# Kernel tuning notes

Hardware: AMD Instinct MI355X
Metric: run time of the kernel (lower is better)

Reference implementation:

```python
import math
import jax, jax.numpy as jnp
import numpy as np

E = 1024   # embed_dim
H = 16     # num_heads
DH = E // H
EPS = 1e-8

def round_ste(x):
    # straight-through round (matches brevitas STE behavior)
    return x + jax.lax.stop_gradient(jnp.round(x) - x)

def _scale(x, qmax):
    # dynamic per-tensor abs-max scale (stand-in for brevitas calibrated scale)
    return jnp.maximum(jnp.max(jnp.abs(x)) / qmax, EPS)

def fq(x, s, qmin, qmax):
    # fake-quantize: quantize to int grid, dequantize back to float
    return jnp.clip(round_ste(x / s), qmin, qmax) * s

def quant_linear(x, W, b):
    # Int8ActPerTensorFloat input, Int8WeightPerTensorFloat (narrow range) weight, Int32Bias
    s_x = _scale(x, 128.0)
    s_w = _scale(W, 127.0)
    xq = fq(x, s_x, -128, 127)
    wq = fq(W, s_w, -127, 127)
    y = xq @ wq.T
    if b is not None:
        s_b = s_x * s_w
        y = y + round_ste(b / s_b) * s_b
    return y

def setup_inputs() -> dict:
    k = jax.random.key(0)
    ks = jax.random.split(k, 7)
    S, B = 1024, 4
    return {
        "query": jax.random.normal(ks[0], (S, B, E), jnp.float32),
        "key": jax.random.normal(ks[1], (S, B, E), jnp.float32),
        "value": jax.random.normal(ks[2], (S, B, E), jnp.float32),
        "in_proj_weight": jax.random.normal(ks[3], (3 * E, E), jnp.float32) * 0.02,
        "in_proj_bias": jax.random.normal(ks[4], (3 * E,), jnp.float32) * 0.02,
        "out_proj_weight": jax.random.normal(ks[5], (E, E), jnp.float32) * 0.02,
        "out_proj_bias": jax.random.normal(ks[6], (E,), jnp.float32) * 0.02,
    }

def reference(query, key, value, in_proj_weight, in_proj_bias, out_proj_weight, out_proj_bias):
    S, B, _ = query.shape
    Wq, Wk, Wv = jnp.split(in_proj_weight, 3, axis=0)
    bq, bk, bv = jnp.split(in_proj_bias, 3)
    # quantized QKV projections (packed in_proj split per-input)
    q = quant_linear(query, Wq, bq)   # (S,B,E)
    k = quant_linear(key, Wk, bk)
    v = quant_linear(value, Wv, bv)

    def to_heads(x):  # (S,B,E) -> (B*H, S, DH)
        return x.reshape(S, B * H, DH).transpose(1, 0, 2)

    q = to_heads(q)
    k = to_heads(k)
    v = to_heads(v)

    # q_scaled quant (int8)
    q = q / math.sqrt(DH)
    q = fq(q, _scale(q, 128.0), -128, 127)
    # k_transposed quant (int8)
    kt = k.transpose(0, 2, 1)  # (B*H, DH, S)
    kt = fq(kt, _scale(kt, 128.0), -128, 127)

    attn = q @ kt                      # (B*H, S, S); softmax_input_quant=None -> identity
    attn = jax.nn.softmax(attn, axis=-1)
    # attn_output_weights quant (uint8)
    s_a = jnp.maximum(jnp.max(attn) / 255.0, EPS)
    attn = jnp.clip(round_ste(attn / s_a), 0, 255) * s_a
    # v quant (int8)
    v = fq(v, _scale(v, 128.0), -128, 127)

    out = attn @ v                     # (B*H, S, DH)
    out = out.transpose(1, 0, 2).reshape(S, B, E)
    out = quant_linear(out, out_proj_weight, out_proj_bias)
    return out
```

## Files before the change

### kernel.cpp

```cpp
#include <hip/hip_runtime.h>
#include <stdint.h>

typedef unsigned short u16;
typedef signed char i8;
typedef unsigned char u8;
typedef __attribute__((ext_vector_type(8))) short bf16x8;
typedef __attribute__((ext_vector_type(4))) float f32x4;
typedef __attribute__((ext_vector_type(4))) int i32x4;

#define S_LEN 1024
#define BATCH 4
#define EMB   1024
#define NH    16
#define DHEAD 64
#define BHEAD 64
#define NTOK  4096
#define KDIM  1024
#define NDIM  1024
#define EPSF  1e-8f
#define LOG2E 1.4426950408889634f

#define MFMAI8(a,b,c)  __builtin_amdgcn_mfma_i32_16x16x64_i8((a),(b),(c),0,0,0)

#define GLOAD16(g, l) __builtin_amdgcn_global_load_lds( \
    (const __attribute__((address_space(1))) void*)(g), \
    (__attribute__((address_space(3))) void*)(l), 16, 0, 0)

#define EXP2F(x) __builtin_amdgcn_exp2f(x)

__device__ __forceinline__ unsigned pack4(float a, float b, float c, float d){
  int qa = (int)a, qb = (int)b, qc = (int)c, qd = (int)d;
  return (unsigned)(qa & 255) | ((unsigned)(qb & 255) << 8) |
         ((unsigned)(qc & 255) << 16) | ((unsigned)(qd & 255) << 24);
}

__device__ __forceinline__ float wave_max(float v){
#pragma unroll
  for (int off = 32; off > 0; off >>= 1) v = fmaxf(v, __shfl_xor(v, off));
  return v;
}


__global__ __launch_bounds__(256) void k_zero(float* sc, int* vtot){
  if (blockIdx.x == 0){
    if (threadIdx.x < 16) sc[threadIdx.x] = 0.0f;
  } else {
    vtot[(blockIdx.x - 1)*256 + threadIdx.x] = 0;
  }
}

struct AQDesc { const float* x; u8* y; int n4; int slot; float qdiv; float lo; };
struct AQTable { AQDesc d[7]; };

__global__ __launch_bounds__(256) void k_absmax7(AQTable t, int* __restrict__ sci){
  const int bid = blockIdx.x;
  int seg, b0, nb;
  if (bid < 1536){ seg = bid >> 9; b0 = seg << 9; nb = 512; }
  else { seg = 3 + ((bid - 1536) >> 7); b0 = 1536 + ((seg - 3) << 7); nb = 128; }
  const AQDesc D = t.d[seg];
  float m = 0.0f;
  const float4* x4 = (const float4*)D.x;
  for (int i = (bid - b0)*256 + threadIdx.x; i < D.n4; i += nb*256){
    float4 v = x4[i];
    m = fmaxf(m, fmaxf(fmaxf(fabsf(v.x), fabsf(v.y)), fmaxf(fabsf(v.z), fabsf(v.w))));
  }
  m = wave_max(m);
  __shared__ float red[4];
  int lane = threadIdx.x & 63, w = threadIdx.x >> 6;
  if (lane == 0) red[w] = m;
  __syncthreads();
  if (threadIdx.x == 0){
    float mm = fmaxf(fmaxf(red[0], red[1]), fmaxf(red[2], red[3]));
    atomicMax(sci + D.slot, __float_as_int(mm));
  }
}

__global__ __launch_bounds__(256) void k_quant7(AQTable t, const float* __restrict__ sc){
  const int bid = blockIdx.x;
  int seg, b0, nb;
  if (bid < 1536){ seg = bid >> 9; b0 = seg << 9; nb = 512; }
  else { seg = 3 + ((bid - 1536) >> 7); b0 = 1536 + ((seg - 3) << 7); nb = 128; }
  const AQDesc D = t.d[seg];
  const float s = fmaxf(sc[D.slot] / D.qdiv, EPSF);
  const float lo = D.lo;
  const float4* x4 = (const float4*)D.x;
  unsigned* y4 = (unsigned*)D.y;
  for (int i = (bid - b0)*256 + threadIdx.x; i < D.n4; i += nb*256){
    float4 v = x4[i];
    float t0 = fminf(fmaxf(rintf(v.x / s), lo), 127.f);
    float t1 = fminf(fmaxf(rintf(v.y / s), lo), 127.f);
    float t2 = fminf(fmaxf(rintf(v.z / s), lo), 127.f);
    float t3 = fminf(fmaxf(rintf(v.w / s), lo), 127.f);
    y4[i] = pack4(t0, t1, t2, t3);
  }
}

__global__ __launch_bounds__(256) void k_quant(const float* __restrict__ x,
    u8* __restrict__ y, int n4, const float* __restrict__ sc, int slot){
  const float s = fmaxf(sc[slot] / 128.0f, EPSF);
  const float4* x4 = (const float4*)x;
  unsigned* y4 = (unsigned*)y;
  for (int i = blockIdx.x*256 + threadIdx.x; i < n4; i += gridDim.x*256){
    float4 v = x4[i];
    float t0 = fminf(fmaxf(rintf(v.x / s), -128.f), 127.f);
    float t1 = fminf(fmaxf(rintf(v.y / s), -128.f), 127.f);
    float t2 = fminf(fmaxf(rintf(v.z / s), -128.f), 127.f);
    float t3 = fminf(fmaxf(rintf(v.w / s), -128.f), 127.f);
    y4[i] = pack4(t0, t1, t2, t3);
  }
}

__device__ __forceinline__ void gemm_body(const i8* __restrict__ A,
    const i8* __restrict__ W, const float* __restrict__ bias,
    float* __restrict__ out, float s_b, int rowBase, int colBase,
    int* __restrict__ amax_out, i8 (*As)[128], i8 (*Bs)[128], float* red){
  const int tid = threadIdx.x;
  const int wid = tid >> 6, lane = tid & 63;
  const int wm = wid >> 2, wn = wid & 3;
  const int rr = lane & 15, g = lane >> 4;
  const int srow = wid*8 + (lane >> 3);
  const int sco  = ((lane & 7) ^ (lane >> 3)) << 4;
  const i8* Arow0 = &A[(size_t)(rowBase + srow)*KDIM + sco];
  const i8* Arow1 = &A[(size_t)(rowBase + 64 + srow)*KDIM + sco];
  const i8* Wrow0 = &W[(size_t)(colBase + srow)*KDIM + sco];
  const i8* Wrow1 = &W[(size_t)(colBase + 64 + srow)*KDIM + sco];
  i32x4 c[4][2] = {};
  int aoff[4][2], boff[2][2];
#pragma unroll
  for (int i = 0; i < 4; i++){
    int row = wm*64 + i*16 + rr;
#pragma unroll
    for (int h = 0; h < 2; h++)
      aoff[i][h] = row*128 + (((h*4 + g) ^ (row & 7)) << 4);
  }
#pragma unroll
  for (int j = 0; j < 2; j++){
    int row = wn*32 + j*16 + rr;
#pragma unroll
    for (int h = 0; h < 2; h++)
      boff[j][h] = row*128 + (((h*4 + g) ^ (row & 7)) << 4);
  }
  for (int k0 = 0; k0 < KDIM; k0 += 128){
    __syncthreads();
    GLOAD16(Arow0 + k0, &As[wid*8][0]);
    GLOAD16(Arow1 + k0, &As[64 + wid*8][0]);
    GLOAD16(Wrow0 + k0, &Bs[wid*8][0]);
    GLOAD16(Wrow1 + k0, &Bs[64 + wid*8][0]);
    __syncthreads();
#pragma unroll
    for (int h = 0; h < 2; h++){
      i32x4 af[4], bfr[2];
#pragma unroll
      for (int i = 0; i < 4; i++) af[i]  = *(const i32x4*)((const i8*)As + aoff[i][h]);
#pragma unroll
      for (int j = 0; j < 2; j++) bfr[j] = *(const i32x4*)((const i8*)Bs + boff[j][h]);
#pragma unroll
      for (int i = 0; i < 4; i++)
#pragma unroll
        for (int j = 0; j < 2; j++)
          c[i][j] = MFMAI8(af[i], bfr[j], c[i][j]);
    }
  }
  float lmax = 0.0f;
  const int r0 = (lane >> 4) * 4, ccol = lane & 15;
#pragma unroll
  for (int j = 0; j < 2; j++){
    int col = colBase + wn*32 + j*16 + ccol;
    float rb = rintf(bias[col] / s_b);
#pragma unroll
    for (int i = 0; i < 4; i++){
      int rowb = rowBase + wm*64 + i*16 + r0;
#pragma unroll
      for (int rI = 0; rI < 4; rI++){
        float y = s_b * ((float)c[i][j][rI] + rb);
        out[(size_t)(rowb + rI)*NDIM + col] = y;
        lmax = fmaxf(lmax, fabsf(y));
      }
    }
  }
  lmax = wave_max(lmax);
  if (lane == 0) red[wid] = lmax;
  __syncthreads();
  if (tid == 0){
    float mm = red[0];
#pragma unroll
    for (int i2 = 1; i2 < 8; i2++) mm = fmaxf(mm, red[i2]);
    atomicMax(amax_out, __float_as_int(mm));
  }
}

__global__ __launch_bounds__(512) void k_gemm3(const i8* __restrict__ Xall,
    const i8* __restrict__ Wall, const float* __restrict__ ball,
    float* __restrict__ Yall, const float* __restrict__ sc, int* __restrict__ sci){
  __shared__ i8 As[128][128];
  __shared__ i8 Bs[128][128];
  __shared__ float red[8];
  const int orig = blockIdx.x;
  const int xcd = orig & 7, sl = orig >> 3;
  const int seg = sl >> 5;
  const int t2 = xcd*32 + (sl & 31);
  const int by = t2 >> 3, bx = t2 & 7;
  const float s_x = fmaxf(sc[seg] / 128.0f, EPSF);
  const float s_w = fmaxf(sc[3 + seg] / 127.0f, EPSF);
  gemm_body(Xall + (size_t)seg*NTOK*KDIM, Wall + (size_t)seg*KDIM*NDIM,
            ball + seg*1024, Yall + (size_t)seg*NTOK*NDIM, s_x*s_w,
            by*128, bx*128, sci + 7 + seg, As, Bs, red);
}

__global__ __launch_bounds__(512) void k_gemm1(const i8* __restrict__ A,
    const i8* __restrict__ W, const float* __restrict__ bias,
    float* __restrict__ out, const float* __restrict__ sc,
    int sx_slot, int sw_slot, int* __restrict__ amax_out){
  __shared__ i8 As[128][128];
  __shared__ i8 Bs[128][128];
  __shared__ float red[8];
  const int orig = blockIdx.x;
  const int t2 = (orig & 7)*32 + (orig >> 3);
  const int by = t2 >> 3, bx = t2 & 7;
  const float s_x = fmaxf(sc[sx_slot] / 128.0f, EPSF);
  const float s_w = fmaxf(sc[sw_slot] / 127.0f, EPSF);
  gemm_body(A, W, bias, out, s_x*s_w, by*128, bx*128, amax_out, As, Bs, red);
}

__global__ __launch_bounds__(256) void k_quant_heads(const float* __restrict__ qf,
    const float* __restrict__ kf, const float* __restrict__ vf,
    i8* __restrict__ qh, i8* __restrict__ kh, i8* __restrict__ vt,
    int* __restrict__ vtot, const float* __restrict__ sc){
  const float s_q = fmaxf((sc[7]*0.125f)/128.0f, EPSF);
  const float s_k = fmaxf(sc[8]/128.0f, EPSF);
  const float s_v = fmaxf(sc[9]/128.0f, EPSF);
  __shared__ i8 tile[64][68];
  const int bx = blockIdx.x;
  const int st = bx & 15, hh = (bx >> 4) & 15, b = bx >> 8;
  const int t = threadIdx.x;
  const int sl = t >> 2, dc = (t & 3) * 16;
  const size_t row = (size_t)(st*64 + sl)*BATCH + b;
  const size_t ibase = row*EMB + hh*DHEAD + dc;
  const int bh = b*NH + hh;
  float vq[16], vk[16], vv[16];
#pragma unroll
  for (int i = 0; i < 4; i++){
    *(float4*)&vq[i*4] = *(const float4*)&qf[ibase + i*4];
    *(float4*)&vk[i*4] = *(const float4*)&kf[ibase + i*4];
    *(float4*)&vv[i*4] = *(const float4*)&vf[ibase + i*4];
  }
  alignas(16) i8 oq[16], ok[16];
#pragma unroll
  for (int i = 0; i < 16; i++){
    float tq = fminf(fmaxf(rintf((vq[i]*0.125f)/s_q), -128.f), 127.f);
    float tk = fminf(fmaxf(rintf(vk[i]/s_k), -128.f), 127.f);
    float tv = fminf(fmaxf(rintf(vv[i]/s_v), -128.f), 127.f);
    oq[i] = (i8)(int)tq; ok[i] = (i8)(int)tk;
    tile[dc + i][sl] = (i8)(int)tv;
  }
  const size_t qoff = ((size_t)bh*S_LEN + st*64 + sl)*DHEAD + dc;
  *(int4*)&qh[qoff] = *(const int4*)&oq[0];
  *(int4*)&kh[qoff] = *(const int4*)&ok[0];
  __syncthreads();
  const int d = t >> 2, sc4 = (t & 3) * 16;
  int ovi[4];
  int sum = 0;
#pragma unroll
  for (int w4 = 0; w4 < 4; w4++){
    unsigned x = *(const unsigned*)&tile[d][sc4 + w4*4];
    ovi[w4] = (int)x;
#pragma unroll
    for (int bb = 0; bb < 4; bb++) sum += (int)(i8)(x >> (8*bb));
  }
  const size_t voff = ((size_t)bh*DHEAD + d)*S_LEN + st*64 + sc4;
  *(int4*)&vt[voff] = *(const int4*)&ovi[0];
  sum += __shfl_xor(sum, 1);
  sum += __shfl_xor(sum, 2);
  if ((t & 3) == 0) atomicAdd(&vtot[bh*DHEAD + d], sum);
}

__global__ __launch_bounds__(256) void k_attn1(const i8* __restrict__ qh,
    const i8* __restrict__ kh, float* __restrict__ mrow, float* __restrict__ lrow,
    const float* __restrict__ sc, int* __restrict__ sci){
  __shared__ i8 Ks[64][64];
  __shared__ float red2[4];
  const int orig = blockIdx.x;
  const int tile = (orig & 7) * 128 + (orig >> 3);
  const int bhead = tile >> 4, q0 = (tile & 15) * 64;
  const int tid = threadIdx.x, w = tid >> 6, lane = tid & 63;
  const int rr = lane & 15, g = lane >> 4;
  const float s_q = fmaxf((sc[7]*0.125f)/128.0f, EPSF);
  const float s_k = fmaxf(sc[8]/128.0f, EPSF);
  const float C1 = s_q * s_k * LOG2E;
  const i8* qbase = qh + ((size_t)bhead*S_LEN + q0 + w*16)*DHEAD;
  const i8* kbase = kh + (size_t)bhead*S_LEN*DHEAD;
  i32x4 a = *(const i32x4*)&qbase[rr*DHEAD + g*16];
  const int srow = w*16 + (lane >> 2);
  const int sco  = ((lane & 3) ^ ((srow >> 1) & 3)) << 4;
  float m[4] = {-1e30f, -1e30f, -1e30f, -1e30f};
  float l[4] = {0.f, 0.f, 0.f, 0.f};
  for (int cch = 0; cch < 16; cch++){
    const int n0 = cch * 64;
    __syncthreads();
    GLOAD16(&kbase[(size_t)(n0 + srow)*DHEAD + sco], &Ks[w*16][0]);
    __syncthreads();
    float sv[4][4];
#pragma unroll
    for (int nt = 0; nt < 4; nt++){
      int row = nt*16 + rr;
      i32x4 b = *(const i32x4*)((const i8*)Ks + row*64 + (((g ^ ((row >> 1) & 3))) << 4));
      i32x4 acc = {};
      acc = MFMAI8(a, b, acc);
#pragma unroll
      for (int r = 0; r < 4; r++) sv[nt][r] = (float)acc[r]*C1;
    }
#pragma unroll
    for (int r = 0; r < 4; r++){
      float cm = fmaxf(fmaxf(sv[0][r], sv[1][r]), fmaxf(sv[2][r], sv[3][r]));
      float mn = fmaxf(m[r], cm);
      l[r] *= EXP2F(m[r] - mn);
      m[r] = mn;
#pragma unroll
      for (int nt = 0; nt < 4; nt++)
        l[r] += EXP2F(sv[nt][r] - m[r]);
    }
  }
#pragma unroll
  for (int off = 1; off < 16; off <<= 1){
#pragma unroll
    for (int r = 0; r < 4; r++){
      float mo = __shfl_xor(m[r], off), lo = __shfl_xor(l[r], off);
      float mn = fmaxf(m[r], mo);
      l[r] = l[r]*EXP2F(m[r] - mn) + lo*EXP2F(mo - mn);
      m[r] = mn;
    }
  }
  if (rr == 0){
    int rowb = q0 + w*16 + g*4;
#pragma unroll
    for (int r = 0; r < 4; r++){
      mrow[(size_t)bhead*S_LEN + rowb + r] = m[r];
      lrow[(size_t)bhead*S_LEN + rowb + r] = l[r];
    }
  }
  float im = 0.0f;
#pragma unroll
  for (int r = 0; r < 4; r++) im = fmaxf(im, 1.0f / l[r]);
  im = wave_max(im);
  if (lane == 0) red2[w] = im;
  __syncthreads();
  if (tid == 0){
    float mm = fmaxf(fmaxf(red2[0], red2[1]), fmaxf(red2[2], red2[3]));
    atomicMax(sci + 13, __float_as_int(mm));
  }
}

__global__ __launch_bounds__(256) void k_attn2(const i8* __restrict__ qh,
    const i8* __restrict__ kh, const i8* __restrict__ vt,
    const float* __restrict__ mrow, const float* __restrict__ lrow,
    const int* __restrict__ vtot, float* __restrict__ aout,
    const float* __restrict__ sc, const int* __restrict__ sci,
    int* __restrict__ amax_out){
  __shared__ i8 Ks[64][64];
  __shared__ i8 Vs[64][64];
  __shared__ i8 P[4][16][68];
  __shared__ float red[4];
  const int orig = blockIdx.x;
  const int tile = (orig & 7) * 128 + (orig >> 3);
  const int bhead = tile >> 4, q0 = (tile & 15) * 64;
  const int tid = threadIdx.x, w = tid >> 6, lane = tid & 63;
  const int rr = lane & 15, g = lane >> 4;
  const float s_q = fmaxf((sc[7]*0.125f)/128.0f, EPSF);
  const float s_k = fmaxf(sc[8]/128.0f, EPSF);
  const float C1 = s_q * s_k * LOG2E;
  const float s_v = fmaxf(sc[9]/128.0f, EPSF);
  const float s_a = fmaxf(__int_as_float(sci[13]) / 255.0f, EPSF);
  const float fac = s_a * s_v;
  const i8* qbase = qh + ((size_t)bhead*S_LEN + q0 + w*16)*DHEAD;
  const i8* kbase = kh + (size_t)bhead*S_LEN*DHEAD;
  const i8* vbase = vt + (size_t)bhead*DHEAD*S_LEN;
  i32x4 a = *(const i32x4*)&qbase[rr*DHEAD + g*16];
  float nm[4], inv[4];
  {
    int rowb = q0 + w*16 + g*4;
#pragma unroll
    for (int r = 0; r < 4; r++){
      nm[r]  = -mrow[(size_t)bhead*S_LEN + rowb + r];
      inv[r] = 1.0f / (lrow[(size_t)bhead*S_LEN + rowb + r] * s_a);
    }
  }
  const int srow = w*16 + (lane >> 2);
  const int sco  = ((lane & 3) ^ ((srow >> 1) & 3)) << 4;
  const int vco  = (lane & 3) << 4;
  i32x4 cpv[4] = {};
  for (int cch = 0; cch < 16; cch++){
    const int n0 = cch * 64;
    __syncthreads();
    GLOAD16(&kbase[(size_t)(n0 + srow)*DHEAD + sco], &Ks[w*16][0]);
    GLOAD16(&vbase[(size_t)srow*S_LEN + n0 + vco], &Vs[w*16][0]);
    __syncthreads();
#pragma unroll
    for (int nt = 0; nt < 4; nt++){
      int row = nt*16 + rr;
      i32x4 b = *(const i32x4*)((const i8*)Ks + row*64 + (((g ^ ((row >> 1) & 3))) << 4));
      i32x4 acc = {};
      acc = MFMAI8(a, b, acc);
#pragma unroll
      for (int r = 0; r < 4; r++){
        float arg = fmaf((float)acc[r], C1, nm[r]);
        float e   = EXP2F(arg);
        float pq  = fminf(rintf(e * inv[r]), 255.0f);
        P[w][g*4 + r][nt*16 + rr] = (i8)((int)pq - 128);
      }
    }
    i32x4 pa;
    {
      const i8* pptr = &P[w][rr][g*16];
      pa[0] = *(const int*)(pptr + 0);
      pa[1] = *(const int*)(pptr + 4);
      pa[2] = *(const int*)(pptr + 8);
      pa[3] = *(const int*)(pptr + 12);
    }
#pragma unroll
    for (int f = 0; f < 4; f++){
      i32x4 bv = *(const i32x4*)&Vs[f*16 + rr][g*16];
      cpv[f] = MFMAI8(pa, bv, cpv[f]);
    }
  }
  const int b = bhead >> 4, hh = bhead & 15;
  float lmax = 0.0f;
#pragma unroll
  for (int f = 0; f < 4; f++){
    int d = f*16 + rr;
    int vcorr = 128 * vtot[bhead*DHEAD + d];
#pragma unroll
    for (int r = 0; r < 4; r++){
      int srow2 = q0 + w*16 + g*4 + r;
      float y = fac * (float)(cpv[f][r] + vcorr);
      aout[(size_t)(srow2*BATCH + b)*EMB + hh*DHEAD + d] = y;
      lmax = fmaxf(lmax, fabsf(y));
    }
  }
  lmax = wave_max(lmax);
  __syncthreads();
  if (lane == 0) red[w] = lmax;
  __syncthreads();
  if (tid == 0){
    float mm = fmaxf(fmaxf(red[0], red[1]), fmaxf(red[2], red[3]));
    atomicMax(amax_out, __float_as_int(mm));
  }
}

extern "C" void kernel_launch(void* const* d_in, const int* in_sizes, int n_in,
                              void* d_out, int out_size, void* d_ws, size_t ws_size,
                              hipStream_t stream){
  const float* query = (const float*)d_in[0];
  const float* key   = (const float*)d_in[1];
  const float* value = (const float*)d_in[2];
  const float* inW   = (const float*)d_in[3];
  const float* inB   = (const float*)d_in[4];
  const float* outW  = (const float*)d_in[5];
  const float* outB  = (const float*)d_in[6];
  float* out = (float*)d_out;

  char* ws = (char*)d_ws;
  float* sc  = (float*)ws;
  int*   sci = (int*)ws;
  int*   vtotI = (int*)(ws + 256);
  u8* WQQ = (u8*)(ws + 256 + 16384);
  u8* WKQ = WQQ + 1024*1024;
  u8* WVQ = WKQ + 1024*1024;
  u8* WOQ = WVQ + 1024*1024;
  u8* XQ  = WOQ + 1024*1024;
  u8* XK  = XQ + (size_t)NTOK*1024;
  u8* XV  = XK + (size_t)NTOK*1024;
  float* QF = (float*)(XV + (size_t)NTOK*1024);
  float* KF = QF + (size_t)NTOK*1024;
  float* VF = KF + (size_t)NTOK*1024;
  i8* VT = (i8*)(VF + (size_t)NTOK*1024);
  float* MROW = (float*)(VT + (size_t)BHEAD*DHEAD*S_LEN);
  float* LROW = MROW + BHEAD*S_LEN;
  i8* QH  = (i8*)XQ;   i8* KH = (i8*)XK;
  float* AOUT = QF;
  u8* AOQ = XV;

  AQTable tab;
  tab.d[0] = { query,             XQ,  NTOK*1024/4, 0, 128.f, -128.f };
  tab.d[1] = { key,               XK,  NTOK*1024/4, 1, 128.f, -128.f };
  tab.d[2] = { value,             XV,  NTOK*1024/4, 2, 128.f, -128.f };
  tab.d[3] = { inW,               WQQ, 1024*1024/4, 3, 127.f, -127.f };
  tab.d[4] = { inW + 1024*1024,   WKQ, 1024*1024/4, 4, 127.f, -127.f };
  tab.d[5] = { inW + 2*1024*1024, WVQ, 1024*1024/4, 5, 127.f, -127.f };
  tab.d[6] = { outW,              WOQ, 1024*1024/4, 6, 127.f, -127.f };

  k_zero<<<17, 256, 0, stream>>>(sc, vtotI);
  k_absmax7<<<2048, 256, 0, stream>>>(tab, sci);
  k_quant7<<<2048, 256, 0, stream>>>(tab, sc);
  k_gemm3<<<768, 512, 0, stream>>>((const i8*)XQ, (const i8*)WQQ, inB, QF, sc, sci);
  k_quant_heads<<<1024, 256, 0, stream>>>(QF, KF, VF, QH, KH, VT, vtotI, sc);
  k_attn1<<<1024, 256, 0, stream>>>(QH, KH, MROW, LROW, sc, sci);
  k_attn2<<<1024, 256, 0, stream>>>(QH, KH, VT, MROW, LROW, vtotI, AOUT, sc, sci, sci + 10);
  k_quant<<<1024, 256, 0, stream>>>(AOUT, AOQ, NTOK*1024/4, sc, 10);
  k_gemm1<<<256, 512, 0, stream>>>((const i8*)AOQ, (const i8*)WOQ, outB, out, sc, 10, 6, sci + 12);
}
```

Baseline: 191.6 us.

## Transpose QK MFMA operands so each lane owns one query row, pack P writes

The attention kernels swap the MFMA operand order so each lane holds scores for a single query row. Softmax stats then reduce across lane groups with shuffles instead of keeping four rows per lane. In the second pass, the normalization is folded into the exp2 bias via log2(inv). The four uint8 probabilities are packed into one 32-bit shared store with a single XOR for the offset, and the V tile in LDS gets an XOR swizzle to reduce bank conflicts. The exp-then-scale is approximated by exp2 with a log-folded bias, which could shift rounding slightly at the quantization edges.

```diff
diff --git a/kernel.cpp b/kernel.cpp
--- a/kernel.cpp
+++ b/kernel.cpp
@@ -292,8 +292,7 @@
   i32x4 a = *(const i32x4*)&qbase[rr*DHEAD + g*16];
   const int srow = w*16 + (lane >> 2);
   const int sco  = ((lane & 3) ^ ((srow >> 1) & 3)) << 4;
-  float m[4] = {-1e30f, -1e30f, -1e30f, -1e30f};
-  float l[4] = {0.f, 0.f, 0.f, 0.f};
+  float m = -1e30f, l = 0.0f;
   for (int cch = 0; cch < 16; cch++){
     const int n0 = cch * 64;
     __syncthreads();
@@ -305,43 +304,35 @@
       int row = nt*16 + rr;
       i32x4 b = *(const i32x4*)((const i8*)Ks + row*64 + (((g ^ ((row >> 1) & 3))) << 4));
       i32x4 acc = {};
-      acc = MFMAI8(a, b, acc);
+      acc = MFMAI8(b, a, acc);
 #pragma unroll
       for (int r = 0; r < 4; r++) sv[nt][r] = (float)acc[r]*C1;
     }
-#pragma unroll
-    for (int r = 0; r < 4; r++){
-      float cm = fmaxf(fmaxf(sv[0][r], sv[1][r]), fmaxf(sv[2][r], sv[3][r]));
-      float mn = fmaxf(m[r], cm);
-      l[r] *= EXP2F(m[r] - mn);
-      m[r] = mn;
-#pragma unroll
-      for (int nt = 0; nt < 4; nt++)
-        l[r] += EXP2F(sv[nt][r] - m[r]);
-    }
-  }
-#pragma unroll
-  for (int off = 1; off < 16; off <<= 1){
-#pragma unroll
-    for (int r = 0; r < 4; r++){
-      float mo = __shfl_xor(m[r], off), lo = __shfl_xor(l[r], off);
-      float mn = fmaxf(m[r], mo);
-      l[r] = l[r]*EXP2F(m[r] - mn) + lo*EXP2F(mo - mn);
-      m[r] = mn;
-    }
-  }
-  if (rr == 0){
-    int rowb = q0 + w*16 + g*4;
-#pragma unroll
-    for (int r = 0; r < 4; r++){
-      mrow[(size_t)bhead*S_LEN + rowb + r] = m[r];
-      lrow[(size_t)bhead*S_LEN + rowb + r] = l[r];
-    }
-  }
-  float im = 0.0f;
-#pragma unroll
-  for (int r = 0; r < 4; r++) im = fmaxf(im, 1.0f / l[r]);
-  im = wave_max(im);
+    float cm = sv[0][0];
+#pragma unroll
+    for (int nt = 0; nt < 4; nt++)
+#pragma unroll
+      for (int r = 0; r < 4; r++) cm = fmaxf(cm, sv[nt][r]);
+    float mn = fmaxf(m, cm);
+    l *= EXP2F(m - mn);
+    m = mn;
+#pragma unroll
+    for (int nt = 0; nt < 4; nt++)
+#pragma unroll
+      for (int r = 0; r < 4; r++) l += EXP2F(sv[nt][r] - m);
+  }
+#pragma unroll
+  for (int off = 16; off < 64; off <<= 1){
+    float mo = __shfl_xor(m, off), lo = __shfl_xor(l, off);
+    float mn = fmaxf(m, mo);
+    l = l*EXP2F(m - mn) + lo*EXP2F(mo - mn);
+    m = mn;
+  }
+  if (g == 0){
+    mrow[(size_t)bhead*S_LEN + q0 + w*16 + rr] = m;
+    lrow[(size_t)bhead*S_LEN + q0 + w*16 + rr] = l;
+  }
+  float im = wave_max(1.0f / l);
   if (lane == 0) red2[w] = im;
   __syncthreads();
   if (tid == 0){
@@ -375,18 +366,15 @@
   const i8* kbase = kh + (size_t)bhead*S_LEN*DHEAD;
   const i8* vbase = vt + (size_t)bhead*DHEAD*S_LEN;
   i32x4 a = *(const i32x4*)&qbase[rr*DHEAD + g*16];
-  float nm[4], inv[4];
+  float nb;
   {
-    int rowb = q0 + w*16 + g*4;
-#pragma unroll
-    for (int r = 0; r < 4; r++){
-      nm[r]  = -mrow[(size_t)bhead*S_LEN + rowb + r];
-      inv[r] = 1.0f / (lrow[(size_t)bhead*S_LEN + rowb + r] * s_a);
-    }
+    size_t qr = (size_t)bhead*S_LEN + q0 + w*16 + rr;
+    float inv = 1.0f / (lrow[qr] * s_a);
+    nb = log2f(inv) - mrow[qr];
   }
   const int srow = w*16 + (lane >> 2);
   const int sco  = ((lane & 3) ^ ((srow >> 1) & 3)) << 4;
-  const int vco  = (lane & 3) << 4;
+  const int vco  = ((lane & 3) ^ (srow & 3)) << 4;
   i32x4 cpv[4] = {};
   for (int cch = 0; cch < 16; cch++){
     const int n0 = cch * 64;
@@ -399,14 +387,16 @@
       int row = nt*16 + rr;
       i32x4 b = *(const i32x4*)((const i8*)Ks + row*64 + (((g ^ ((row >> 1) & 3))) << 4));
       i32x4 acc = {};
-      acc = MFMAI8(a, b, acc);
+      acc = MFMAI8(b, a, acc);
+      unsigned pw = 0;
 #pragma unroll
       for (int r = 0; r < 4; r++){
-        float arg = fmaf((float)acc[r], C1, nm[r]);
-        float e   = EXP2F(arg);
-        float pq  = fminf(rintf(e * inv[r]), 255.0f);
-        P[w][g*4 + r][nt*16 + rr] = (i8)((int)pq - 128);
+        float e  = EXP2F(fmaf((float)acc[r], C1, nb));
+        int   pq = (int)fminf(rintf(e), 255.0f);
+        pw |= (unsigned)pq << (8*r);
       }
+      pw ^= 0x80808080u;
+      *(unsigned*)&P[w][rr][nt*16 + g*4] = pw;
     }
     i32x4 pa;
     {
@@ -418,7 +408,8 @@
     }
 #pragma unroll
     for (int f = 0; f < 4; f++){
-      i32x4 bv = *(const i32x4*)&Vs[f*16 + rr][g*16];
+      int row = f*16 + rr;
+      i32x4 bv = *(const i32x4*)((const i8*)Vs + row*64 + (((g ^ (row & 3))) << 4));
       cpv[f] = MFMAI8(pa, bv, cpv[f]);
     }
   }
```

Result: faster. 186.2 us (-2.8%).
